# Kernel tuning notes

Measured on AMD Instinct MI355X. Metric: run time of the kernel, lower is better.

The kernel has to match this reference:

```python
import jax, jax.numpy as jnp
import numpy as np

EPS = 1e-8  # CosineSimilarity eps
T = 0.5     # temperature


def _neg_indices(B):
    # static boolean mask removing diag and +/-B off-diagonals, as flat indices
    N = 2 * B
    m = np.eye(N) + np.eye(N, k=B) + np.eye(N, k=-B)
    mask = (1 - m).astype(bool)
    return np.nonzero(mask.ravel())[0]  # shape [N*(N-2)]


def setup_inputs() -> dict:
    key = jax.random.key(0)
    k1, k2 = jax.random.split(key)
    B, D = 4096, 128
    proj_i = jax.random.normal(k1, (B, D), dtype=jnp.float32)
    proj_j = jax.random.normal(k2, (B, D), dtype=jnp.float32)
    return {"proj_i": proj_i, "proj_j": proj_j}


def reference(proj_i, proj_j):
    B = proj_i.shape[0]
    N = 2 * B
    p = jnp.concatenate([proj_i, proj_j], axis=0)  # [N, D]
    # cosine sim of normalized vectors == dot product of unit vectors
    z = p / jnp.maximum(jnp.linalg.norm(p, axis=1, keepdims=True), EPS)
    sim = z @ z.T  # [N, N]
    pos = jnp.concatenate([jnp.diagonal(sim, offset=B), jnp.diagonal(sim, offset=-B)])  # [N]
    neg_idx = jnp.asarray(_neg_indices(B))
    neg = sim.ravel()[neg_idx].reshape(N, N - 2)
    logits = jnp.concatenate([pos[:, None], neg], axis=1) / T  # [N, N-1]
    # cross-entropy with label 0, sum reduction, divided by N
    logp = jax.nn.log_softmax(logits, axis=-1)
    loss = -jnp.sum(logp[:, 0]) / N
    return loss
```

## Files before the change

### kernel.cpp

```cpp
#include <hip/hip_runtime.h>
#include <hip/hip_bf16.h>

typedef __attribute__((ext_vector_type(8))) short short8;
typedef __attribute__((ext_vector_type(4))) float f32x4;

#define N_TOT 8192
#define HALF_B 4096
#define D 128
#define BM 128
#define BN 128
#define NQ 8
#define SLICE (N_TOT / NQ)
#define NSTEP (SLICE / BN)
#define SCALE 1.6986437f
#define LN2 0.69314718f

#if __has_builtin(__builtin_amdgcn_exp2f)
  #define EXP2(x) __builtin_amdgcn_exp2f(x)
#else
  #define EXP2(x) exp2f(x)
#endif

static __device__ inline unsigned short f2bf(float f) {
    unsigned int u = __builtin_bit_cast(unsigned int, f);
    u = (u + 0x7fffu + ((u >> 16) & 1u)) >> 16;
    return (unsigned short)u;
}
static __device__ inline float bf2f(unsigned int b) {
    return __builtin_bit_cast(float, b << 16);
}

static __device__ __forceinline__ void gload16(const void* g, void* l) {
    __builtin_amdgcn_global_load_lds(
        (const __attribute__((address_space(1))) unsigned int*)g,
        (__attribute__((address_space(3))) unsigned int*)l, 16, 0, 0);
}

static __device__ __forceinline__ void stage_tile(const unsigned short* __restrict__ z,
                                                  int src_row, char* ldsbase, int tid) {
    int wv = tid >> 6, ln = tid & 63;
    const char* zb = (const char*)z;
    #pragma unroll
    for (int i = 0; i < 8; ++i) {
        int L  = wv * 8192 + i * 1024;
        int Ll = L + ln * 16;
        int r  = Ll >> 8;
        int c2 = (Ll & 255) ^ ((r & 7) << 4);
        gload16(zb + (size_t)(src_row + r) * 256 + c2, ldsbase + L);
    }
}

static __device__ __forceinline__ short8 ldsfrag(const char* ldsbase, int row, int kbyte) {
    int off = row * 256 + (kbyte ^ ((row & 7) << 4));
    return *reinterpret_cast<const short8*>(ldsbase + off);
}

__global__ __launch_bounds__(256) void nrm_k(const float* __restrict__ pi,
                                             const float* __restrict__ pj,
                                             unsigned short* __restrict__ z) {
    int row  = (int)(blockIdx.x * 4) + (int)(threadIdx.x >> 6);
    int lane = (int)threadIdx.x & 63;
    const float* src = (row < HALF_B) ? (pi + (size_t)row * D)
                                      : (pj + (size_t)(row - HALF_B) * D);
    float2 v = *reinterpret_cast<const float2*>(src + lane * 2);
    float ss = v.x * v.x + v.y * v.y;
    #pragma unroll
    for (int off = 32; off >= 1; off >>= 1) ss += __shfl_xor(ss, off);
    float inv = SCALE / fmaxf(sqrtf(ss), 1e-8f);
    unsigned int packed = ((unsigned int)f2bf(v.y * inv) << 16) | (unsigned int)f2bf(v.x * inv);
    *reinterpret_cast<unsigned int*>(z + (size_t)row * D + lane * 2) = packed;
}

__global__ __launch_bounds__(256, 2) void sim_k(const unsigned short* __restrict__ z,
                                                float* __restrict__ s_part) {
    __shared__ char lds[64 * 1024];
    char* Asm = lds;
    char* Bsm = lds + 32768;

    int tid  = (int)threadIdx.x;
    int lane = tid & 63;
    int wid  = tid >> 6;
    int lr   = lane & 15;
    int kg   = lane >> 4;
    int R0   = (int)blockIdx.x * BM;
    int C0   = (int)blockIdx.y * SLICE;

    stage_tile(z, R0, Asm, tid);
    stage_tile(z, C0, Bsm, tid);
    __syncthreads();

    short8 a[2][4];
    #pragma unroll
    for (int m = 0; m < 2; ++m)
        #pragma unroll
        for (int kt = 0; kt < 4; ++kt)
            a[m][kt] = ldsfrag(Asm, wid * 32 + m * 16 + lr, kg * 16 + kt * 64);

    float s[2][4];
    #pragma unroll
    for (int m = 0; m < 2; ++m)
        #pragma unroll
        for (int r = 0; r < 4; ++r) s[m][r] = 0.0f;

    for (int bs = 0; bs < NSTEP; ++bs) {
        if (bs) {
            __syncthreads();
            stage_tile(z, C0 + bs * BN, Bsm, tid);
            __syncthreads();
        }
        #pragma unroll
        for (int nt = 0; nt < 8; ++nt) {
            short8 b[4];
            #pragma unroll
            for (int kt = 0; kt < 4; ++kt)
                b[kt] = ldsfrag(Bsm, nt * 16 + lr, kg * 16 + kt * 64);
            #pragma unroll
            for (int m = 0; m < 2; ++m) {
                f32x4 acc = {0.0f, 0.0f, 0.0f, 0.0f};
                #pragma unroll
                for (int kt = 0; kt < 4; ++kt)
                    acc = __builtin_amdgcn_mfma_f32_16x16x32_bf16(a[m][kt], b[kt], acc, 0, 0, 0);
                #pragma unroll
                for (int r = 0; r < 4; ++r)
                    s[m][r] += EXP2(acc[r]);
            }
        }
    }

    #pragma unroll
    for (int off = 1; off <= 8; off <<= 1)
        #pragma unroll
        for (int m = 0; m < 2; ++m)
            #pragma unroll
            for (int r = 0; r < 4; ++r)
                s[m][r] += __shfl_xor(s[m][r], off);

    if (lr == 0) {
        int rowbase = R0 + wid * 32;
        #pragma unroll
        for (int m = 0; m < 2; ++m)
            #pragma unroll
            for (int r = 0; r < 4; ++r)
                s_part[(size_t)(rowbase + m * 16 + kg * 4 + r) * NQ + blockIdx.y] = s[m][r];
    }
}

__global__ __launch_bounds__(256) void red1_k(const unsigned short* __restrict__ z,
                                              const float* __restrict__ s_part,
                                              float* __restrict__ partial) {
    int wid  = (int)threadIdx.x >> 6;
    int lane = (int)threadIdx.x & 63;
    int row  = (int)blockIdx.x * 4 + wid;

    float S = (lane < NQ) ? s_part[(size_t)row * NQ + lane] : 0.0f;

    unsigned int ua = *reinterpret_cast<const unsigned int*>(z + (size_t)row * D + lane * 2);
    unsigned int ub = *reinterpret_cast<const unsigned int*>(z + (size_t)(row ^ HALF_B) * D + lane * 2);
    float a0 = bf2f(ua & 0xffffu), a1 = bf2f(ua >> 16);
    float b0 = bf2f(ub & 0xffffu), b1 = bf2f(ub >> 16);
    float dacc = a0 * a0 + a1 * a1;
    float pacc = a0 * b0 + a1 * b1;

    #pragma unroll
    for (int off = 32; off >= 1; off >>= 1) {
        S    += __shfl_xor(S, off);
        dacc += __shfl_xor(dacc, off);
        pacc += __shfl_xor(pacc, off);
    }
    float Li = __logf(S - EXP2(dacc)) - pacc * LN2;

    __shared__ float ls[4];
    if (lane == 0) ls[wid] = Li;
    __syncthreads();
    if (threadIdx.x == 0)
        partial[blockIdx.x] = ls[0] + ls[1] + ls[2] + ls[3];
}

__global__ __launch_bounds__(1024) void red2_k(const float* __restrict__ partial,
                                               float* __restrict__ out) {
    int tid = (int)threadIdx.x;
    float v = partial[tid] + partial[tid + 1024];
    #pragma unroll
    for (int off = 32; off >= 1; off >>= 1) v += __shfl_xor(v, off);
    __shared__ float ls[16];
    if ((tid & 63) == 0) ls[tid >> 6] = v;
    __syncthreads();
    if (tid < 16) {
        float w = ls[tid];
        #pragma unroll
        for (int off = 8; off >= 1; off >>= 1) w += __shfl_xor(w, off);
        if (tid == 0) out[0] = w * (1.0f / (float)N_TOT);
    }
}

extern "C" void kernel_launch(void* const* d_in, const int* in_sizes, int n_in,
                              void* d_out, int out_size, void* d_ws, size_t ws_size,
                              hipStream_t stream) {
    const float* pi = (const float*)d_in[0];
    const float* pj = (const float*)d_in[1];
    float* out = (float*)d_out;

    unsigned short* z = (unsigned short*)d_ws;
    float* s_part = (float*)((char*)d_ws + (size_t)N_TOT * D * 2);
    float* partial = s_part + (size_t)N_TOT * NQ;

    nrm_k<<<dim3(N_TOT / 4), dim3(256), 0, stream>>>(pi, pj, z);
    sim_k<<<dim3(N_TOT / BM, NQ), dim3(256), 0, stream>>>(z, s_part);
    red1_k<<<dim3(N_TOT / 4), dim3(256), 0, stream>>>(z, s_part, partial);
    red2_k<<<dim3(1), dim3(1024), 0, stream>>>(partial, out);
}
```

Baseline: 33.13 us.

## Exploit symmetry of similarity matrix to skip lower-triangle column slices

```diff
diff --git a/kernel.cpp b/kernel.cpp
--- a/kernel.cpp
+++ b/kernel.cpp
@@ -12,6 +12,7 @@
 #define NQ 8
 #define SLICE (N_TOT / NQ)
 #define NSTEP (SLICE / BN)
+#define NSLOT 64
 #define SCALE 1.6986437f
 #define LN2 0.69314718f
 
@@ -73,17 +74,23 @@
 
 __global__ __launch_bounds__(256, 2) void sim_k(const unsigned short* __restrict__ z,
                                                 float* __restrict__ s_part) {
+    int bi = (int)blockIdx.x;
+    int cq = (int)blockIdx.y;
+    if (cq < (bi >> 3)) return;
+    bool em = (cq > (bi >> 3));
+
     __shared__ char lds[64 * 1024];
     char* Asm = lds;
     char* Bsm = lds + 32768;
+    float* colbuf = (float*)lds;
 
     int tid  = (int)threadIdx.x;
     int lane = tid & 63;
     int wid  = tid >> 6;
     int lr   = lane & 15;
     int kg   = lane >> 4;
-    int R0   = (int)blockIdx.x * BM;
-    int C0   = (int)blockIdx.y * SLICE;
+    int R0   = bi * BM;
+    int C0   = cq * SLICE;
 
     stage_tile(z, R0, Asm, tid);
     stage_tile(z, C0, Bsm, tid);
@@ -95,6 +102,7 @@
         #pragma unroll
         for (int kt = 0; kt < 4; ++kt)
             a[m][kt] = ldsfrag(Asm, wid * 32 + m * 16 + lr, kg * 16 + kt * 64);
+    __syncthreads();
 
     float s[2][4];
     #pragma unroll
@@ -114,6 +122,7 @@
             #pragma unroll
             for (int kt = 0; kt < 4; ++kt)
                 b[kt] = ldsfrag(Bsm, nt * 16 + lr, kg * 16 + kt * 64);
+            float cs = 0.0f;
             #pragma unroll
             for (int m = 0; m < 2; ++m) {
                 f32x4 acc = {0.0f, 0.0f, 0.0f, 0.0f};
@@ -121,8 +130,17 @@
                 for (int kt = 0; kt < 4; ++kt)
                     acc = __builtin_amdgcn_mfma_f32_16x16x32_bf16(a[m][kt], b[kt], acc, 0, 0, 0);
                 #pragma unroll
-                for (int r = 0; r < 4; ++r)
-                    s[m][r] += EXP2(acc[r]);
+                for (int r = 0; r < 4; ++r) {
+                    float ev = EXP2(acc[r]);
+                    s[m][r] += ev;
+                    cs += ev;
+                }
+            }
+            if (em) {
+                cs += __shfl_xor(cs, 16);
+                cs += __shfl_xor(cs, 32);
+                if (kg == 0)
+                    colbuf[wid * 1024 + bs * 128 + nt * 16 + lr] = cs;
             }
         }
     }
@@ -141,7 +159,22 @@
         for (int m = 0; m < 2; ++m)
             #pragma unroll
             for (int r = 0; r < 4; ++r)
-                s_part[(size_t)(rowbase + m * 16 + kg * 4 + r) * NQ + blockIdx.y] = s[m][r];
+                s_part[(size_t)(rowbase + m * 16 + kg * 4 + r) * NSLOT + cq] = s[m][r];
+    }
+
+    if (em) {
+        __syncthreads();
+        #pragma unroll
+        for (int u = 0; u < 4; ++u) {
+            int col = tid * 4 + (u & 3);
+        }
+        int c0 = tid * 4;
+        #pragma unroll
+        for (int u = 0; u < 4; ++u) {
+            int col = c0 + u;
+            float v = colbuf[col] + colbuf[1024 + col] + colbuf[2048 + col] + colbuf[3072 + col];
+            s_part[(size_t)(C0 + col) * NSLOT + 8 + bi] = v;
+        }
     }
 }
 
@@ -151,8 +184,10 @@
     int wid  = (int)threadIdx.x >> 6;
     int lane = (int)threadIdx.x & 63;
     int row  = (int)blockIdx.x * 4 + wid;
-
-    float S = (lane < NQ) ? s_part[(size_t)row * NQ + lane] : 0.0f;
+    int g    = row >> 10;
+
+    bool valid = (lane < 8) ? (lane >= g) : ((lane - 8) < (g << 3));
+    float S = valid ? s_part[(size_t)row * NSLOT + lane] : 0.0f;
 
     unsigned int ua = *reinterpret_cast<const unsigned int*>(z + (size_t)row * D + lane * 2);
     unsigned int ub = *reinterpret_cast<const unsigned int*>(z + (size_t)(row ^ HALF_B) * D + lane * 2);
@@ -202,7 +237,7 @@
 
     unsigned short* z = (unsigned short*)d_ws;
     float* s_part = (float*)((char*)d_ws + (size_t)N_TOT * D * 2);
-    float* partial = s_part + (size_t)N_TOT * NQ;
+    float* partial = s_part + (size_t)N_TOT * NSLOT;
 
     nrm_k<<<dim3(N_TOT / 4), dim3(256), 0, stream>>>(pi, pj, z);
     sim_k<<<dim3(N_TOT / BM, NQ), dim3(256), 0, stream>>>(z, s_part);
```

Result: slower. 43.81 us (+32.2%).

## Double-buffer B tiles and switch sim kernel to 32x32x16 MFMA

Applied to the files above, without the earlier changes.

```diff
diff --git a/kernel.cpp b/kernel.cpp
--- a/kernel.cpp
+++ b/kernel.cpp
@@ -2,13 +2,13 @@
 #include <hip/hip_bf16.h>
 
 typedef __attribute__((ext_vector_type(8))) short short8;
-typedef __attribute__((ext_vector_type(4))) float f32x4;
+typedef __attribute__((ext_vector_type(16))) float f32x16;
 
 #define N_TOT 8192
 #define HALF_B 4096
 #define D 128
 #define BM 128
-#define BN 128
+#define BN 64
 #define NQ 8
 #define SLICE (N_TOT / NQ)
 #define NSTEP (SLICE / BN)
@@ -36,22 +36,25 @@
         (__attribute__((address_space(3))) unsigned int*)l, 16, 0, 0);
 }
 
-static __device__ __forceinline__ void stage_tile(const unsigned short* __restrict__ z,
+template<int ROWS>
+static __device__ __forceinline__ void stage_rows(const unsigned short* __restrict__ z,
                                                   int src_row, char* ldsbase, int tid) {
     int wv = tid >> 6, ln = tid & 63;
     const char* zb = (const char*)z;
-    #pragma unroll
-    for (int i = 0; i < 8; ++i) {
-        int L  = wv * 8192 + i * 1024;
+    constexpr int per_wave = ROWS * 256 / 4;
+    constexpr int chunks = per_wave / 1024;
+    #pragma unroll
+    for (int i = 0; i < chunks; ++i) {
+        int L  = wv * per_wave + i * 1024;
         int Ll = L + ln * 16;
         int r  = Ll >> 8;
-        int c2 = (Ll & 255) ^ ((r & 7) << 4);
+        int c2 = (Ll & 255) ^ ((r & 15) << 4);
         gload16(zb + (size_t)(src_row + r) * 256 + c2, ldsbase + L);
     }
 }
 
 static __device__ __forceinline__ short8 ldsfrag(const char* ldsbase, int row, int kbyte) {
-    int off = row * 256 + (kbyte ^ ((row & 7) << 4));
+    int off = row * 256 + (kbyte ^ ((row & 15) << 4));
     return *reinterpret_cast<const short8*>(ldsbase + off);
 }
 
@@ -75,73 +78,64 @@
                                                 float* __restrict__ s_part) {
     __shared__ char lds[64 * 1024];
     char* Asm = lds;
-    char* Bsm = lds + 32768;
+    char* B0  = lds + 32768;
+    char* B1  = lds + 49152;
 
     int tid  = (int)threadIdx.x;
     int lane = tid & 63;
     int wid  = tid >> 6;
-    int lr   = lane & 15;
-    int kg   = lane >> 4;
+    int lrow = lane & 31;
+    int kh   = lane >> 5;
     int R0   = (int)blockIdx.x * BM;
     int C0   = (int)blockIdx.y * SLICE;
 
-    stage_tile(z, R0, Asm, tid);
-    stage_tile(z, C0, Bsm, tid);
+    stage_rows<128>(z, R0, Asm, tid);
+    stage_rows<64>(z, C0, B0, tid);
     __syncthreads();
 
-    short8 a[2][4];
-    #pragma unroll
-    for (int m = 0; m < 2; ++m)
-        #pragma unroll
-        for (int kt = 0; kt < 4; ++kt)
-            a[m][kt] = ldsfrag(Asm, wid * 32 + m * 16 + lr, kg * 16 + kt * 64);
-
-    float s[2][4];
-    #pragma unroll
-    for (int m = 0; m < 2; ++m)
-        #pragma unroll
-        for (int r = 0; r < 4; ++r) s[m][r] = 0.0f;
-
+    short8 a[8];
+    #pragma unroll
+    for (int ks = 0; ks < 8; ++ks)
+        a[ks] = ldsfrag(Asm, wid * 32 + lrow, ks * 32 + kh * 16);
+
+    float s[16];
+    #pragma unroll
+    for (int r = 0; r < 16; ++r) s[r] = 0.0f;
+
+    char* Bcur = B0;
+    char* Bnxt = B1;
     for (int bs = 0; bs < NSTEP; ++bs) {
-        if (bs) {
-            __syncthreads();
-            stage_tile(z, C0 + bs * BN, Bsm, tid);
-            __syncthreads();
+        if (bs + 1 < NSTEP)
+            stage_rows<64>(z, C0 + (bs + 1) * BN, Bnxt, tid);
+        #pragma unroll
+        for (int ct = 0; ct < 2; ++ct) {
+            f32x16 acc;
+            #pragma unroll
+            for (int r = 0; r < 16; ++r) acc[r] = 0.0f;
+            #pragma unroll
+            for (int ks = 0; ks < 8; ++ks) {
+                short8 b = ldsfrag(Bcur, ct * 32 + lrow, ks * 32 + kh * 16);
+                acc = __builtin_amdgcn_mfma_f32_32x32x16_bf16(a[ks], b, acc, 0, 0, 0);
+            }
+            #pragma unroll
+            for (int r = 0; r < 16; ++r)
+                s[r] += EXP2(acc[r]);
         }
-        #pragma unroll
-        for (int nt = 0; nt < 8; ++nt) {
-            short8 b[4];
-            #pragma unroll
-            for (int kt = 0; kt < 4; ++kt)
-                b[kt] = ldsfrag(Bsm, nt * 16 + lr, kg * 16 + kt * 64);
-            #pragma unroll
-            for (int m = 0; m < 2; ++m) {
-                f32x4 acc = {0.0f, 0.0f, 0.0f, 0.0f};
-                #pragma unroll
-                for (int kt = 0; kt < 4; ++kt)
-                    acc = __builtin_amdgcn_mfma_f32_16x16x32_bf16(a[m][kt], b[kt], acc, 0, 0, 0);
-                #pragma unroll
-                for (int r = 0; r < 4; ++r)
-                    s[m][r] += EXP2(acc[r]);
-            }
-        }
-    }
-
-    #pragma unroll
-    for (int off = 1; off <= 8; off <<= 1)
-        #pragma unroll
-        for (int m = 0; m < 2; ++m)
-            #pragma unroll
-            for (int r = 0; r < 4; ++r)
-                s[m][r] += __shfl_xor(s[m][r], off);
-
-    if (lr == 0) {
-        int rowbase = R0 + wid * 32;
-        #pragma unroll
-        for (int m = 0; m < 2; ++m)
-            #pragma unroll
-            for (int r = 0; r < 4; ++r)
-                s_part[(size_t)(rowbase + m * 16 + kg * 4 + r) * NQ + blockIdx.y] = s[m][r];
+        __syncthreads();
+        char* t = Bcur; Bcur = Bnxt; Bnxt = t;
+    }
+
+    #pragma unroll
+    for (int off = 1; off <= 16; off <<= 1)
+        #pragma unroll
+        for (int r = 0; r < 16; ++r)
+            s[r] += __shfl_xor(s[r], off);
+
+    if (lrow == 0) {
+        int rb = R0 + wid * 32 + kh * 4;
+        #pragma unroll
+        for (int r = 0; r < 16; ++r)
+            s_part[(size_t)(rb + (r & 3) + 8 * (r >> 2)) * NQ + blockIdx.y] = s[r];
     }
 }
 
```

Result: slower. 35.83 us (+8.1%).

## Fuse row reductions into sim kernel with fixed-point atomics and last-block finalize

Applied to the files above, without the earlier changes.

```diff
diff --git a/kernel.cpp b/kernel.cpp
--- a/kernel.cpp
+++ b/kernel.cpp
@@ -13,7 +13,10 @@
 #define SLICE (N_TOT / NQ)
 #define NSTEP (SLICE / BN)
 #define SCALE 1.6986437f
-#define LN2 0.69314718f
+#define CDIAG 7.3890561f
+#define S_SC  1099511627776.0f
+#define INV_S_SC (1.0 / 1099511627776.0)
+#define L_SC  1048576.0
 
 #if __has_builtin(__builtin_amdgcn_exp2f)
   #define EXP2(x) __builtin_amdgcn_exp2f(x)
@@ -25,9 +28,6 @@
     unsigned int u = __builtin_bit_cast(unsigned int, f);
     u = (u + 0x7fffu + ((u >> 16) & 1u)) >> 16;
     return (unsigned short)u;
-}
-static __device__ inline float bf2f(unsigned int b) {
-    return __builtin_bit_cast(float, b << 16);
 }
 
 static __device__ __forceinline__ void gload16(const void* g, void* l) {
@@ -57,22 +57,51 @@
 
 __global__ __launch_bounds__(256) void nrm_k(const float* __restrict__ pi,
                                              const float* __restrict__ pj,
-                                             unsigned short* __restrict__ z) {
-    int row  = (int)(blockIdx.x * 4) + (int)(threadIdx.x >> 6);
-    int lane = (int)threadIdx.x & 63;
-    const float* src = (row < HALF_B) ? (pi + (size_t)row * D)
-                                      : (pj + (size_t)(row - HALF_B) * D);
-    float2 v = *reinterpret_cast<const float2*>(src + lane * 2);
-    float ss = v.x * v.x + v.y * v.y;
-    #pragma unroll
-    for (int off = 32; off >= 1; off >>= 1) ss += __shfl_xor(ss, off);
-    float inv = SCALE / fmaxf(sqrtf(ss), 1e-8f);
-    unsigned int packed = ((unsigned int)f2bf(v.y * inv) << 16) | (unsigned int)f2bf(v.x * inv);
-    *reinterpret_cast<unsigned int*>(z + (size_t)row * D + lane * 2) = packed;
-}
-
-__global__ __launch_bounds__(256, 2) void sim_k(const unsigned short* __restrict__ z,
-                                                float* __restrict__ s_part) {
+                                             unsigned short* __restrict__ z,
+                                             float* __restrict__ ppos,
+                                             unsigned long long* __restrict__ S64,
+                                             unsigned int* __restrict__ done,
+                                             unsigned long long* __restrict__ loss64,
+                                             unsigned int* __restrict__ gdone) {
+    int tid = (int)threadIdx.x;
+    if (blockIdx.x < 64) {
+        ((unsigned int*)S64)[blockIdx.x * 256 + tid] = 0u;
+    } else if (blockIdx.x == 64) {
+        if (tid < 64) done[tid] = 0u;
+        else if (tid == 64) *gdone = 0u;
+        else if (tid < 67) ((unsigned int*)loss64)[tid - 65] = 0u;
+    }
+
+    int wid = tid >> 6, lane = tid & 63;
+    int r = (int)blockIdx.x * 4 + wid;
+    float2 va = *reinterpret_cast<const float2*>(pi + (size_t)r * D + lane * 2);
+    float2 vb = *reinterpret_cast<const float2*>(pj + (size_t)r * D + lane * 2);
+    float ssa = va.x * va.x + va.y * va.y;
+    float ssb = vb.x * vb.x + vb.y * vb.y;
+    float sab = va.x * vb.x + va.y * vb.y;
+    #pragma unroll
+    for (int off = 32; off >= 1; off >>= 1) {
+        ssa += __shfl_xor(ssa, off);
+        ssb += __shfl_xor(ssb, off);
+        sab += __shfl_xor(sab, off);
+    }
+    float na = fmaxf(sqrtf(ssa), 1e-8f);
+    float nb = fmaxf(sqrtf(ssb), 1e-8f);
+    float inva = SCALE / na, invb = SCALE / nb;
+    unsigned int pa = ((unsigned int)f2bf(va.y * inva) << 16) | (unsigned int)f2bf(va.x * inva);
+    unsigned int pb = ((unsigned int)f2bf(vb.y * invb) << 16) | (unsigned int)f2bf(vb.x * invb);
+    *reinterpret_cast<unsigned int*>(z + (size_t)r * D + lane * 2) = pa;
+    *reinterpret_cast<unsigned int*>(z + (size_t)(r + HALF_B) * D + lane * 2) = pb;
+    if (lane == 0) ppos[r] = 2.0f * sab / (na * nb);
+}
+
+__global__ __launch_bounds__(256, 2) void simfin_k(const unsigned short* __restrict__ z,
+                                                   const float* __restrict__ ppos,
+                                                   unsigned long long* __restrict__ S64,
+                                                   unsigned int* __restrict__ done,
+                                                   unsigned long long* __restrict__ loss64,
+                                                   unsigned int* __restrict__ gdone,
+                                                   float* __restrict__ out) {
     __shared__ char lds[64 * 1024];
     char* Asm = lds;
     char* Bsm = lds + 32768;
@@ -82,7 +111,8 @@
     int wid  = tid >> 6;
     int lr   = lane & 15;
     int kg   = lane >> 4;
-    int R0   = (int)blockIdx.x * BM;
+    int bi   = (int)blockIdx.x;
+    int R0   = bi * BM;
     int C0   = (int)blockIdx.y * SLICE;
 
     stage_tile(z, R0, Asm, tid);
@@ -141,55 +171,39 @@
         for (int m = 0; m < 2; ++m)
             #pragma unroll
             for (int r = 0; r < 4; ++r)
-                s_part[(size_t)(rowbase + m * 16 + kg * 4 + r) * NQ + blockIdx.y] = s[m][r];
-    }
-}
-
-__global__ __launch_bounds__(256) void red1_k(const unsigned short* __restrict__ z,
-                                              const float* __restrict__ s_part,
-                                              float* __restrict__ partial) {
-    int wid  = (int)threadIdx.x >> 6;
-    int lane = (int)threadIdx.x & 63;
-    int row  = (int)blockIdx.x * 4 + wid;
-
-    float S = (lane < NQ) ? s_part[(size_t)row * NQ + lane] : 0.0f;
-
-    unsigned int ua = *reinterpret_cast<const unsigned int*>(z + (size_t)row * D + lane * 2);
-    unsigned int ub = *reinterpret_cast<const unsigned int*>(z + (size_t)(row ^ HALF_B) * D + lane * 2);
-    float a0 = bf2f(ua & 0xffffu), a1 = bf2f(ua >> 16);
-    float b0 = bf2f(ub & 0xffffu), b1 = bf2f(ub >> 16);
-    float dacc = a0 * a0 + a1 * a1;
-    float pacc = a0 * b0 + a1 * b1;
-
-    #pragma unroll
-    for (int off = 32; off >= 1; off >>= 1) {
-        S    += __shfl_xor(S, off);
-        dacc += __shfl_xor(dacc, off);
-        pacc += __shfl_xor(pacc, off);
-    }
-    float Li = __logf(S - EXP2(dacc)) - pacc * LN2;
-
-    __shared__ float ls[4];
-    if (lane == 0) ls[wid] = Li;
-    __syncthreads();
-    if (threadIdx.x == 0)
-        partial[blockIdx.x] = ls[0] + ls[1] + ls[2] + ls[3];
-}
-
-__global__ __launch_bounds__(1024) void red2_k(const float* __restrict__ partial,
-                                               float* __restrict__ out) {
-    int tid = (int)threadIdx.x;
-    float v = partial[tid] + partial[tid + 1024];
-    #pragma unroll
-    for (int off = 32; off >= 1; off >>= 1) v += __shfl_xor(v, off);
-    __shared__ float ls[16];
-    if ((tid & 63) == 0) ls[tid >> 6] = v;
-    __syncthreads();
-    if (tid < 16) {
-        float w = ls[tid];
-        #pragma unroll
-        for (int off = 8; off >= 1; off >>= 1) w += __shfl_xor(w, off);
-        if (tid == 0) out[0] = w * (1.0f / (float)N_TOT);
+                atomicAdd(&S64[rowbase + m * 16 + kg * 4 + r],
+                          (unsigned long long)(long long)llrintf(s[m][r] * S_SC));
+    }
+    __threadfence();
+    __syncthreads();
+
+    volatile int* flagp = (int*)lds;
+    if (tid == 0) *flagp = (int)atomicAdd(&done[bi], 1u);
+    __syncthreads();
+    if (*flagp != 7) return;
+    __threadfence();
+
+    float Li = 0.0f;
+    if (tid < 128) {
+        int row = R0 + tid;
+        unsigned long long sv = atomicAdd(&S64[row], 0ull);
+        float S = (float)((double)sv * INV_S_SC);
+        Li = __logf(S - CDIAG) - ppos[row & (HALF_B - 1)];
+    }
+    #pragma unroll
+    for (int off = 32; off >= 1; off >>= 1) Li += __shfl_xor(Li, off);
+    float* wp = (float*)(lds + 64);
+    if (lane == 0) wp[wid] = Li;
+    __syncthreads();
+    if (tid == 0) {
+        double tot = (double)wp[0] + (double)wp[1] + (double)wp[2] + (double)wp[3];
+        atomicAdd(loss64, (unsigned long long)(long long)llrint(tot * L_SC));
+        __threadfence();
+        unsigned int og = atomicAdd(gdone, 1u);
+        if (og == 63u) {
+            long long lv = (long long)atomicAdd(loss64, 0ull);
+            out[0] = (float)((double)lv / L_SC / (double)N_TOT);
+        }
     }
 }
 
@@ -200,12 +214,14 @@
     const float* pj = (const float*)d_in[1];
     float* out = (float*)d_out;
 
-    unsigned short* z = (unsigned short*)d_ws;
-    float* s_part = (float*)((char*)d_ws + (size_t)N_TOT * D * 2);
-    float* partial = s_part + (size_t)N_TOT * NQ;
-
-    nrm_k<<<dim3(N_TOT / 4), dim3(256), 0, stream>>>(pi, pj, z);
-    sim_k<<<dim3(N_TOT / BM, NQ), dim3(256), 0, stream>>>(z, s_part);
-    red1_k<<<dim3(N_TOT / 4), dim3(256), 0, stream>>>(z, s_part, partial);
-    red2_k<<<dim3(1), dim3(1024), 0, stream>>>(partial, out);
-}
+    char* ws = (char*)d_ws;
+    unsigned short* z        = (unsigned short*)ws;
+    float* ppos              = (float*)(ws + 2 * 1024 * 1024);
+    unsigned long long* S64  = (unsigned long long*)(ws + 2 * 1024 * 1024 + 16 * 1024);
+    unsigned int* done       = (unsigned int*)((char*)S64 + 64 * 1024);
+    unsigned long long* l64  = (unsigned long long*)((char*)done + 256);
+    unsigned int* gdone      = (unsigned int*)((char*)l64 + 8);
+
+    nrm_k<<<dim3(1024), dim3(256), 0, stream>>>(pi, pj, z, ppos, S64, done, l64, gdone);
+    simfin_k<<<dim3(N_TOT / BM, NQ), dim3(256), 0, stream>>>(z, ppos, S64, done, l64, gdone, out);
+}
```

New measurement: 61.57 us. 85.8% more time.
